# Kernel tuning notes

Hardware: AMD Instinct MI355X
Metric: run time of the kernel (lower is better)

## Reference

```python
import jax, jax.numpy as jnp
import numpy as np

H, DK, DV = 16, 64, 64
DECAY = 0.99
WRITE_STRENGTH = 1.0


def setup_inputs() -> dict:
    key = jax.random.key(0)
    ks = jax.random.split(key, 7)
    B, S, D = 4, 4096, 2048
    sd = 1.0 / np.sqrt(D)
    return {
        "hidden": jax.random.normal(ks[0], (B, S, D), jnp.float32),
        "memory": jax.random.normal(ks[1], (H, DK, DV), jnp.float32) * 0.02,
        "Wk": jax.random.normal(ks[2], (H * DK, D), jnp.float32) * sd,
        "Wv": jax.random.normal(ks[3], (H * DV, D), jnp.float32) * sd,
        "Wq": jax.random.normal(ks[4], (H * DK, D), jnp.float32) * sd,
        "Wg": jax.random.normal(ks[5], (D, D), jnp.float32) * sd,
        "Wo": jax.random.normal(ks[6], (D, H * DV), jnp.float32) * (1.0 / np.sqrt(H * DV)),
    }


def reference(hidden, memory, Wk, Wv, Wq, Wg, Wo):
    B, S, D = hidden.shape
    # projections (Linear, bias=False): x @ W^T
    k = (hidden @ Wk.T).reshape(B, S, H, DK)
    v = (hidden @ Wv.T).reshape(B, S, H, DV)
    q = (hidden @ Wq.T).reshape(B, S, H, DK)
    # read with pre-update memory: r = q^T M
    readout = jnp.einsum('bshk,hkv->bshv', q, memory).reshape(B, S, H * DV)
    # output gate: h' = h + sigmoid(Wg h) * (Wo r)
    gate = jax.nn.sigmoid(hidden @ Wg.T)
    out = hidden + gate * (readout @ Wo.T)
    # decaying outer-product write: M' = lambda*M + rho * sum_i k_i v_i^T
    new_memory = DECAY * memory + WRITE_STRENGTH * jnp.einsum('bshk,bshv->hkv', k, v)
    return out, new_memory
```

## Files before the change

kernel.cpp:

```cpp
#include <hip/hip_runtime.h>
#include <hip/hip_bf16.h>

typedef __attribute__((ext_vector_type(4))) float f32x4;
typedef __bf16 bf16x8 __attribute__((ext_vector_type(8)));

#define TOKENS 16384
#define DIM    2048
#define NKVQ   3072

__device__ __forceinline__ void gload_lds16(const void* g, void* l) {
  __builtin_amdgcn_global_load_lds((const __attribute__((address_space(1))) void*)g,
                                   (__attribute__((address_space(3))) void*)l, 16, 0, 0);
}

__global__ void cast8_kernel(const float* __restrict__ src, __bf16* __restrict__ dst, int n8) {
  int i = blockIdx.x * blockDim.x + threadIdx.x;
  if (i >= n8) return;
  const float4* s = (const float4*)src;
  float4 a = s[2 * i], b = s[2 * i + 1];
  bf16x8 o;
  o[0] = (__bf16)a.x; o[1] = (__bf16)a.y; o[2] = (__bf16)a.z; o[3] = (__bf16)a.w;
  o[4] = (__bf16)b.x; o[5] = (__bf16)b.y; o[6] = (__bf16)b.z; o[7] = (__bf16)b.w;
  ((bf16x8*)dst)[i] = o;
}

__global__ void weff_kernel(const float* __restrict__ Wo, const float* __restrict__ mem,
                            __bf16* __restrict__ Weff) {
  int idx = blockIdx.x * blockDim.x + threadIdx.x;
  int d = idx >> 10, hk = idx & 1023, h = hk >> 6;
  const float* wo = Wo + d * 1024 + h * 64;
  const float* mm = mem + hk * 64;
  float s = 0.f;
  #pragma unroll 8
  for (int v = 0; v < 64; ++v) s += wo[v] * mm[v];
  Weff[idx] = (__bf16)s;
}

__device__ __forceinline__ void gemm256_core(
    const __bf16* __restrict__ A, int lda,
    const __bf16* __restrict__ B, int ldb,
    int m0, int n0, int nt, char* sm, f32x4 acc[8][4]) {

  const int tid = threadIdx.x, lane = tid & 63, wid = tid >> 6;
  const int wr = wid >> 2, wc = wid & 3;
  const int lrow = lane & 15, kc = lane >> 4;

  int offA[8], offB[4];
  #pragma unroll
  for (int m = 0; m < 8; ++m) {
    int u = (wr * 128 + m * 16 + lrow) * 4 + kc;
    offA[m] = (u ^ ((u >> 3) & 7)) << 4;
  }
  #pragma unroll
  for (int n = 0; n < 4; ++n) {
    int u = (wc * 64 + n * 16 + lrow) * 4 + kc;
    offB[n] = ((u ^ ((u >> 3) & 7)) << 4) + 16384;
  }

  const __bf16* pSA[2]; const __bf16* pSB[2];
  #pragma unroll
  for (int s = 0; s < 2; ++s) {
    int U = s * 512 + tid;
    int u = U ^ ((U >> 3) & 7);
    pSA[s] = A + (size_t)(m0 + (u >> 2)) * lda + (u & 3) * 8;
    pSB[s] = B + (size_t)(n0 + (u >> 2)) * ldb + (u & 3) * 8;
  }

#define BARX() asm volatile("s_barrier" ::: "memory")
#define VM8()  asm volatile("s_waitcnt vmcnt(8)" ::: "memory")
#define VM4()  asm volatile("s_waitcnt vmcnt(4)" ::: "memory")
#define VM0()  asm volatile("s_waitcnt vmcnt(0)" ::: "memory")
#define NOVM
#define NOSTAGE
#define STAGE(bb, tt) do { \
    char* sA = sm + (bb) * 32768 + tid * 16; \
    gload_lds16(pSA[0] + (tt) * 32, sA); \
    gload_lds16(pSA[1] + (tt) * 32, sA + 8192); \
    gload_lds16(pSB[0] + (tt) * 32, sA + 16384); \
    gload_lds16(pSB[1] + (tt) * 32, sA + 24576); } while (0)

#define PHASE(bb, STAGES, WAITS) do { \
    const char* bA = sm + (bb) * 32768; \
    bf16x8 av[8], bv[4]; \
    _Pragma("unroll") for (int m = 0; m < 8; ++m) av[m] = *(const bf16x8*)(bA + offA[m]); \
    _Pragma("unroll") for (int n = 0; n < 4; ++n) bv[n] = *(const bf16x8*)(bA + offB[n]); \
    STAGES; \
    __builtin_amdgcn_sched_barrier(0); \
    __builtin_amdgcn_s_setprio(1); \
    _Pragma("unroll") for (int m = 0; m < 8; ++m) \
      _Pragma("unroll") for (int n = 0; n < 4; ++n) \
        acc[m][n] = __builtin_amdgcn_mfma_f32_16x16x32_bf16(av[m], bv[n], acc[m][n], 0, 0, 0); \
    __builtin_amdgcn_s_setprio(0); \
    WAITS; \
    BARX(); } while (0)

  STAGE(0, 0); STAGE(1, 1); STAGE(2, 2);
  VM8(); BARX();

  for (int i = 0; i < (nt >> 2) - 1; ++i) {
    const int t = i << 2;
    PHASE(0, STAGE(3, t + 3), VM8());
    PHASE(1, STAGE(0, t + 4), VM8());
    PHASE(2, STAGE(1, t + 5), VM8());
    PHASE(3, STAGE(2, t + 6), VM8());
  }
  PHASE(0, STAGE(3, nt - 1), VM8());
  PHASE(1, NOSTAGE, VM4());
  PHASE(2, NOSTAGE, VM0());
  PHASE(3, NOSTAGE, NOVM);
#undef PHASE
#undef STAGE
#undef BARX
#undef VM8
#undef VM4
#undef VM0
#undef NOVM
#undef NOSTAGE
}

__global__ void __launch_bounds__(512, 1)
gemm_fused_kernel(const __bf16* __restrict__ Xb, const __bf16* __restrict__ W1,
                  __bf16* __restrict__ Y, __bf16* __restrict__ Gb) {
  __shared__ __attribute__((aligned(16))) char smem[131072];
  const int g = (blockIdx.x & 7) * 160 + (blockIdx.x >> 3);
  const int bm = g / 20, bn = g % 20;
  const int m0 = bm * 256, n0 = bn * 256;
  f32x4 acc[8][4] = {};
  gemm256_core(Xb, DIM, W1, DIM, m0, n0, 64, smem, acc);

  const int tid = threadIdx.x, wid = tid >> 6, lane = tid & 63;
  const int wr = wid >> 2, wc = wid & 3;
  const int crow = (lane >> 4) << 2, ccol = lane & 15;
  if (bn < 12) {
    #pragma unroll
    for (int f = 0; f < 8; ++f) {
      int row = m0 + wr * 128 + f * 16 + crow;
      #pragma unroll
      for (int n = 0; n < 4; ++n) {
        int col = n0 + wc * 64 + n * 16 + ccol;
        #pragma unroll
        for (int j = 0; j < 4; ++j)
          Y[(size_t)(row + j) * NKVQ + col] = (__bf16)acc[f][n][j];
      }
    }
  } else {
    const int c0 = n0 - 3072;
    #pragma unroll
    for (int f = 0; f < 8; ++f) {
      int row = m0 + wr * 128 + f * 16 + crow;
      #pragma unroll
      for (int n = 0; n < 4; ++n) {
        int col = c0 + wc * 64 + n * 16 + ccol;
        #pragma unroll
        for (int j = 0; j < 4; ++j) {
          float gv = 1.0f / (1.0f + __expf(-acc[f][n][j]));
          Gb[(size_t)(row + j) * DIM + col] = (__bf16)gv;
        }
      }
    }
  }
}

__global__ void __launch_bounds__(512, 1)
gemm_read_kernel(const __bf16* __restrict__ Yq, const __bf16* __restrict__ Weff,
                 const __bf16* __restrict__ Gb, const float* __restrict__ hidden,
                 float* __restrict__ out) {
  __shared__ __attribute__((aligned(16))) char smem[131072];
  const int g = (blockIdx.x & 7) * 64 + (blockIdx.x >> 3);
  const int bm = g >> 3, bn = g & 7;
  const int m0 = bm * 256, n0 = bn * 256;
  f32x4 acc[8][4] = {};
  gemm256_core(Yq, NKVQ, Weff, 1024, m0, n0, 32, smem, acc);

  const int tid = threadIdx.x, wid = tid >> 6, lane = tid & 63;
  const int wr = wid >> 2, wc = wid & 3;
  const int crow = (lane >> 4) << 2, ccol = lane & 15;
  #pragma unroll
  for (int f = 0; f < 8; ++f) {
    int row = m0 + wr * 128 + f * 16 + crow;
    #pragma unroll
    for (int n = 0; n < 4; ++n) {
      int col = n0 + wc * 64 + n * 16 + ccol;
      #pragma unroll
      for (int j = 0; j < 4; ++j) {
        size_t idx = (size_t)(row + j) * DIM + col;
        out[idx] = hidden[idx] + (float)Gb[idx] * acc[f][n][j];
      }
    }
  }
}

__global__ void __launch_bounds__(256)
mem_update_kernel(const __bf16* __restrict__ Y, float* __restrict__ part) {
  const int h = blockIdx.x & 15, sp = blockIdx.x >> 4;
  __shared__ __attribute__((aligned(16))) __bf16 KT[64 * 32];
  __shared__ __attribute__((aligned(16))) __bf16 VT[64 * 32];
  const int tid = threadIdx.x, wid = tid >> 6, lane = tid & 63;
  const int lrow = lane & 15, lk = (lane >> 4) * 8;
  const __bf16* Kbase = Y + (size_t)sp * 1024 * NKVQ + h * 64;
  const __bf16* Vbase = Kbase + 1024;
  f32x4 acc[4] = {};
  const int t = tid >> 3, c8 = (tid & 7) * 8;
  for (int t0 = 0; t0 < 1024; t0 += 32) {
    __syncthreads();
    bf16x8 kv = *(const bf16x8*)(Kbase + (size_t)(t0 + t) * NKVQ + c8);
    bf16x8 vv = *(const bf16x8*)(Vbase + (size_t)(t0 + t) * NKVQ + c8);
    #pragma unroll
    for (int j = 0; j < 8; ++j) {
      KT[(c8 + j) * 32 + t] = kv[j];
      VT[(c8 + j) * 32 + t] = vv[j];
    }
    __syncthreads();
    bf16x8 af = *(const bf16x8*)(KT + (wid * 16 + lrow) * 32 + lk);
    #pragma unroll
    for (int n = 0; n < 4; ++n) {
      bf16x8 bf_ = *(const bf16x8*)(VT + (n * 16 + lrow) * 32 + lk);
      acc[n] = __builtin_amdgcn_mfma_f32_16x16x32_bf16(af, bf_, acc[n], 0, 0, 0);
    }
  }
  float* pp = part + ((size_t)sp * 16 + h) * 4096;
  const int crow = wid * 16 + (lane >> 4) * 4, ccol = lane & 15;
  #pragma unroll
  for (int n = 0; n < 4; ++n)
    #pragma unroll
    for (int r = 0; r < 4; ++r)
      pp[(crow + r) * 64 + n * 16 + ccol] = acc[n][r];
}

__global__ void mem_reduce_kernel(const float* __restrict__ part, const float* __restrict__ mem,
                                  float* __restrict__ out) {
  int i = blockIdx.x * blockDim.x + threadIdx.x;
  float s = 0.99f * mem[i];
  #pragma unroll
  for (int sp = 0; sp < 16; ++sp) s += part[sp * 65536 + i];
  out[i] = s;
}

extern "C" void kernel_launch(void* const* d_in, const int* in_sizes, int n_in,
                              void* d_out, int out_size, void* d_ws, size_t ws_size,
                              hipStream_t stream) {
  const float* hidden = (const float*)d_in[0];
  const float* memory = (const float*)d_in[1];
  const float* Wk = (const float*)d_in[2];
  const float* Wv = (const float*)d_in[3];
  const float* Wq = (const float*)d_in[4];
  const float* Wg = (const float*)d_in[5];
  const float* Wo = (const float*)d_in[6];
  float* out = (float*)d_out;
  float* mem_out = out + (size_t)TOKENS * DIM;

  char* ws = (char*)d_ws;
  __bf16* Xb   = (__bf16*)(ws);
  __bf16* W1   = (__bf16*)(ws + 67108864);
  __bf16* Weff = (__bf16*)(ws + 88080384);
  __bf16* Yb   = (__bf16*)(ws + 92274688);
  __bf16* Gb   = (__bf16*)(ws + 192937984);
  float*  part = (float*)(ws + 260046848);

  cast8_kernel<<<16384, 256, 0, stream>>>(hidden, Xb, 4194304);
  cast8_kernel<<<1024, 256, 0, stream>>>(Wk, W1, 262144);
  cast8_kernel<<<1024, 256, 0, stream>>>(Wv, W1 + 2097152, 262144);
  cast8_kernel<<<1024, 256, 0, stream>>>(Wq, W1 + 4194304, 262144);
  cast8_kernel<<<2048, 256, 0, stream>>>(Wg, W1 + 6291456, 524288);
  weff_kernel<<<8192, 256, 0, stream>>>(Wo, memory, Weff);

  gemm_fused_kernel<<<1280, 512, 0, stream>>>(Xb, W1, Yb, Gb);
  gemm_read_kernel<<<512, 512, 0, stream>>>(Yb + 2048, Weff, Gb, hidden, out);

  mem_update_kernel<<<256, 256, 0, stream>>>(Yb, part);
  mem_reduce_kernel<<<256, 256, 0, stream>>>(part, memory, mem_out);
}
```

Measured before the change: 637.9 us.

## Prefetch next-stage B fragments into registers and use nontemporal epilogue stores

After: 661.1 us. 1.04x slower.

```diff
diff --git a/kernel.cpp b/kernel.cpp
--- a/kernel.cpp
+++ b/kernel.cpp
@@ -11,6 +11,10 @@
 __device__ __forceinline__ void gload_lds16(const void* g, void* l) {
   __builtin_amdgcn_global_load_lds((const __attribute__((address_space(1))) void*)g,
                                    (__attribute__((address_space(3))) void*)l, 16, 0, 0);
+}
+
+__device__ __forceinline__ unsigned short bfbits(float x) {
+  __bf16 b = (__bf16)x; return __builtin_bit_cast(unsigned short, b);
 }
 
 __global__ void cast8_kernel(const float* __restrict__ src, __bf16* __restrict__ dst, int n8) {
@@ -66,8 +70,9 @@
     pSB[s] = B + (size_t)(n0 + (u >> 2)) * ldb + (u & 3) * 8;
   }
 
+  bf16x8 bvS0[4], bvS1[4];
+
 #define BARX() asm volatile("s_barrier" ::: "memory")
-#define VM8()  asm volatile("s_waitcnt vmcnt(8)" ::: "memory")
 #define VM4()  asm volatile("s_waitcnt vmcnt(4)" ::: "memory")
 #define VM0()  asm volatile("s_waitcnt vmcnt(0)" ::: "memory")
 #define NOVM
@@ -79,39 +84,50 @@
     gload_lds16(pSB[0] + (tt) * 32, sA + 16384); \
     gload_lds16(pSB[1] + (tt) * 32, sA + 24576); } while (0)
 
-#define PHASE(bb, STAGES, WAITS) do { \
-    const char* bA = sm + (bb) * 32768; \
-    bf16x8 av[8], bv[4]; \
-    _Pragma("unroll") for (int m = 0; m < 8; ++m) av[m] = *(const bf16x8*)(bA + offA[m]); \
-    _Pragma("unroll") for (int n = 0; n < 4; ++n) bv[n] = *(const bf16x8*)(bA + offB[n]); \
-    STAGES; \
-    __builtin_amdgcn_sched_barrier(0); \
+#define PH(bufC, bufN, C, N, STG, WT) do { \
+    const char* bC = sm + (bufC) * 32768; \
+    const char* bN = sm + (bufN) * 32768; \
+    bf16x8 av[8]; \
+    _Pragma("unroll") for (int m = 0; m < 8; ++m) av[m] = *(const bf16x8*)(bC + offA[m]); \
+    _Pragma("unroll") for (int n = 0; n < 4; ++n) bvS##N[n] = *(const bf16x8*)(bN + offB[n]); \
+    STG; \
     __builtin_amdgcn_s_setprio(1); \
     _Pragma("unroll") for (int m = 0; m < 8; ++m) \
       _Pragma("unroll") for (int n = 0; n < 4; ++n) \
-        acc[m][n] = __builtin_amdgcn_mfma_f32_16x16x32_bf16(av[m], bv[n], acc[m][n], 0, 0, 0); \
+        acc[m][n] = __builtin_amdgcn_mfma_f32_16x16x32_bf16(av[m], bvS##C[n], acc[m][n], 0, 0, 0); \
     __builtin_amdgcn_s_setprio(0); \
-    WAITS; \
-    BARX(); } while (0)
+    WT; BARX(); } while (0)
+
+#define PHF(bufC, C) do { \
+    const char* bC = sm + (bufC) * 32768; \
+    bf16x8 av[8]; \
+    _Pragma("unroll") for (int m = 0; m < 8; ++m) av[m] = *(const bf16x8*)(bC + offA[m]); \
+    __builtin_amdgcn_s_setprio(1); \
+    _Pragma("unroll") for (int m = 0; m < 8; ++m) \
+      _Pragma("unroll") for (int n = 0; n < 4; ++n) \
+        acc[m][n] = __builtin_amdgcn_mfma_f32_16x16x32_bf16(av[m], bvS##C[n], acc[m][n], 0, 0, 0); \
+    __builtin_amdgcn_s_setprio(0); } while (0)
 
   STAGE(0, 0); STAGE(1, 1); STAGE(2, 2);
-  VM8(); BARX();
-
-  for (int i = 0; i < (nt >> 2) - 1; ++i) {
+  VM4(); BARX();
+  #pragma unroll
+  for (int n = 0; n < 4; ++n) bvS0[n] = *(const bf16x8*)(sm + offB[n]);
+
+  for (int i = 0, e = (nt - 4) >> 2; i < e; ++i) {
     const int t = i << 2;
-    PHASE(0, STAGE(3, t + 3), VM8());
-    PHASE(1, STAGE(0, t + 4), VM8());
-    PHASE(2, STAGE(1, t + 5), VM8());
-    PHASE(3, STAGE(2, t + 6), VM8());
-  }
-  PHASE(0, STAGE(3, nt - 1), VM8());
-  PHASE(1, NOSTAGE, VM4());
-  PHASE(2, NOSTAGE, VM0());
-  PHASE(3, NOSTAGE, NOVM);
-#undef PHASE
+    PH(0, 1, 0, 1, STAGE(3, t + 3), VM4());
+    PH(1, 2, 1, 0, STAGE(0, t + 4), VM4());
+    PH(2, 3, 0, 1, STAGE(1, t + 5), VM4());
+    PH(3, 0, 1, 0, STAGE(2, t + 6), VM4());
+  }
+  PH(0, 1, 0, 1, STAGE(3, nt - 1), VM4());
+  PH(1, 2, 1, 0, NOSTAGE, VM0());
+  PH(2, 3, 0, 1, NOSTAGE, NOVM);
+  PHF(3, 1);
+#undef PH
+#undef PHF
 #undef STAGE
 #undef BARX
-#undef VM8
 #undef VM4
 #undef VM0
 #undef NOVM
@@ -140,7 +156,8 @@
         int col = n0 + wc * 64 + n * 16 + ccol;
         #pragma unroll
         for (int j = 0; j < 4; ++j)
-          Y[(size_t)(row + j) * NKVQ + col] = (__bf16)acc[f][n][j];
+          __builtin_nontemporal_store(bfbits(acc[f][n][j]),
+              (unsigned short*)(Y + (size_t)(row + j) * NKVQ + col));
       }
     }
   } else {
@@ -154,7 +171,8 @@
         #pragma unroll
         for (int j = 0; j < 4; ++j) {
           float gv = 1.0f / (1.0f + __expf(-acc[f][n][j]));
-          Gb[(size_t)(row + j) * DIM + col] = (__bf16)gv;
+          __builtin_nontemporal_store(bfbits(gv),
+              (unsigned short*)(Gb + (size_t)(row + j) * DIM + col));
         }
       }
     }
@@ -184,7 +202,8 @@
       #pragma unroll
       for (int j = 0; j < 4; ++j) {
         size_t idx = (size_t)(row + j) * DIM + col;
-        out[idx] = hidden[idx] + (float)Gb[idx] * acc[f][n][j];
+        float v = hidden[idx] + (float)Gb[idx] * acc[f][n][j];
+        __builtin_nontemporal_store(v, out + idx);
       }
     }
   }
```
